# Kernel optimization log

Hardware: AMD Instinct MI355X
Metric: run time of the kernel (lower is better)

The kernel has to match this reference:

```python
import jax, jax.numpy as jnp
import numpy as np

BATCH, T, IN, HID = 64, 2048, 128, 256

def setup_inputs() -> dict:
    key = jax.random.key(0)
    ks = jax.random.split(key, 6)
    s = 0.05
    return {
        "x": jax.random.normal(ks[0], (BATCH, T, IN), dtype=jnp.float32),
        "w_ih0": jax.random.normal(ks[1], (IN, 4 * HID), dtype=jnp.float32) * s,
        "w_hh0": jax.random.normal(ks[2], (HID, 4 * HID), dtype=jnp.float32) * s,
        "b0": jnp.zeros((4 * HID,), dtype=jnp.float32),
        "w_ih1": jax.random.normal(ks[3], (HID, 4 * HID), dtype=jnp.float32) * s,
        "w_hh1": jax.random.normal(ks[4], (HID, 4 * HID), dtype=jnp.float32) * s,
        "b1": jnp.zeros((4 * HID,), dtype=jnp.float32),
    }

def _run_layer(xs, h0, c0, w_ih, w_hh, b):
    # xs: [T, B, D]. Original code iterates input_[T-1-t], i.e. reversed time.
    def step(carry, xt):
        h, c = carry
        gates = xt @ w_ih + h @ w_hh + b            # [B, 4H]
        f, i, o, g = jnp.split(gates, 4, axis=1)     # split order f,i,o,g as in source
        c1 = jax.nn.sigmoid(f) * c + jax.nn.sigmoid(i) * jnp.tanh(g)
        h1 = jax.nn.sigmoid(o) * jnp.tanh(c1)
        return (h1, c1), h1
    (hT, cT), ys = jax.lax.scan(step, (h0, c0), xs[::-1])
    return ys, hT, cT

def reference(x, w_ih0, w_hh0, b0, w_ih1, w_hh1, b1):
    xs = jnp.transpose(x, (1, 0, 2))                 # batch_first -> [T, B, IN]
    B = xs.shape[1]
    H = w_hh0.shape[0]
    h0 = jnp.zeros((B, H), dtype=xs.dtype)
    # Both layers start from the SAME zero hx (faithful to source).
    y0, hn0, cn0 = _run_layer(xs, h0, h0, w_ih0, w_hh0, b0)
    y1, hn1, cn1 = _run_layer(y0, h0, h0, w_ih1, w_hh1, b1)
    # Source never transposes output back: output is [T, B, H]
    return y1, (jnp.stack([hn0, hn1], 0), jnp.stack([cn0, cn1], 0))
```

## Files before the change

### kernel.cpp

```cpp
#include <hip/hip_runtime.h>
#include <cstdint>
#include <cstddef>

#define T_STEPS 2048
#define NBATCH  64
#define HID     256
#define NGATE   1024

#define KR   192
#define KRC  24
#define KLC  8
#define REC_LDS_BYTES (KLC*1024*16 + 1024)

typedef _Float16 f16x8 __attribute__((ext_vector_type(8)));
typedef _Float16 h2f   __attribute__((ext_vector_type(2)));
typedef float    f32x4 __attribute__((ext_vector_type(4)));

__device__ __forceinline__ unsigned short f2h_bits(float f) {
    _Float16 h = (_Float16)f;
    return __builtin_bit_cast(unsigned short, h);
}
__device__ __forceinline__ float h2f_scalar(unsigned short u) {
    return (float)__builtin_bit_cast(_Float16, u);
}

__device__ __forceinline__ float fdot2u(unsigned int hh, unsigned int ww, float acc) {
#if __has_builtin(__builtin_amdgcn_fdot2)
    return __builtin_amdgcn_fdot2(__builtin_bit_cast(h2f, hh),
                                  __builtin_bit_cast(h2f, ww), acc, false);
#else
    h2f a = __builtin_bit_cast(h2f, hh), b = __builtin_bit_cast(h2f, ww);
    return acc + (float)a.x * (float)b.x + (float)a.y * (float)b.y;
#endif
}

#define OFF_G    ((size_t)0)
#define OFF_Y0   ((size_t)268435456)
#define OFF_WT0  ((size_t)335544320)
#define OFF_WT1  ((size_t)336068608)
#define OFF_LW0  ((size_t)336592896)
#define OFF_LW1  ((size_t)336723968)
#define OFF_BS0  ((size_t)336855040)
#define OFF_BS1  ((size_t)337117184)
#define WS_NEED  ((size_t)337641472)

__global__ void convert_weights(const float* __restrict__ w_ih0, const float* __restrict__ w_hh0,
                                const float* __restrict__ w_ih1, const float* __restrict__ w_hh1,
                                unsigned short* __restrict__ WT0, unsigned short* __restrict__ WT1,
                                unsigned short* __restrict__ LW0, unsigned short* __restrict__ LW1,
                                unsigned short* __restrict__ BS0, unsigned short* __restrict__ BS1)
{
    int gid = blockIdx.x * blockDim.x + threadIdx.x;
    int gsz = gridDim.x * blockDim.x;
    for (int s = gid; s < 1024 * 256; s += gsz) {
        int j = s >> 8, k = s & 255;
        WT0[s] = f2h_bits(w_hh0[k * 1024 + j]);
        WT1[s] = f2h_bits(w_hh1[k * 1024 + j]);
    }
    for (int s = gid; s < KLC * 1024 * 8; s += gsz) {
        int i = s & 7, j = (s >> 3) & 1023, c = s >> 13;
        int k = KR + c * 8 + i;
        LW0[s] = f2h_bits(w_hh0[k * 1024 + j]);
        LW1[s] = f2h_bits(w_hh1[k * 1024 + j]);
    }
    for (int s = gid; s < 131072; s += gsz) {
        int i = s & 7, lane = (s >> 3) & 63, kb = (s >> 9) & 3, n16 = s >> 11;
        int k = kb * 32 + (lane >> 4) * 8 + i;
        int n = n16 * 16 + (lane & 15);
        BS0[s] = f2h_bits(w_ih0[k * 1024 + n]);
    }
    for (int s = gid; s < 262144; s += gsz) {
        int i = s & 7, lane = (s >> 3) & 63, kb = (s >> 9) & 7, n16 = s >> 12;
        int k = kb * 32 + (lane >> 4) * 8 + i;
        int n = n16 * 16 + (lane & 15);
        BS1[s] = f2h_bits(w_ih1[k * 1024 + n]);
    }
}

template <int KB, int LAYER>
__global__ __launch_bounds__(256) void gemm_in(const float* __restrict__ A32,
                                               const unsigned short* __restrict__ A16,
                                               const unsigned short* __restrict__ Bsw,
                                               const float* __restrict__ bias,
                                               unsigned short* __restrict__ Gout)
{
    const int lane = threadIdx.x & 63;
    const int wave = threadIdx.x >> 6;
    const int nblk = blockIdx.x & 15;
    const int rblk = blockIdx.x >> 4;
    const int r0 = rblk * 128 + wave * 32;
    const int quad = lane >> 4, ln = lane & 15;

    f32x4 acc[2][4];
#pragma unroll
    for (int q = 0; q < 4; q++) {
        float bv = bias[(nblk * 4 + q) * 16 + ln];
#pragma unroll
        for (int mt = 0; mt < 2; mt++) {
            acc[mt][q][0] = bv; acc[mt][q][1] = bv; acc[mt][q][2] = bv; acc[mt][q][3] = bv;
        }
    }
    const int ar0 = r0 + ln, ar1 = r0 + 16 + ln;
    size_t aoff0, aoff1;
    if (LAYER == 0) {
        aoff0 = ((size_t)(ar0 & 63) * 2048 + (size_t)(2047 - (ar0 >> 6))) * 128;
        aoff1 = ((size_t)(ar1 & 63) * 2048 + (size_t)(2047 - (ar1 >> 6))) * 128;
    } else {
        aoff0 = ((size_t)(2047 - (ar0 >> 6)) * 64 + (size_t)(ar0 & 63)) * 256;
        aoff1 = ((size_t)(2047 - (ar1 >> 6)) * 64 + (size_t)(ar1 & 63)) * 256;
    }
#pragma unroll
    for (int kb = 0; kb < KB; kb++) {
        const int k0 = kb * 32 + quad * 8;
        f16x8 a0, a1;
        if (LAYER == 0) {
            const float* p0 = A32 + aoff0 + k0;
            const float* p1 = A32 + aoff1 + k0;
            float4 fa = *(const float4*)(p0);
            float4 fb = *(const float4*)(p0 + 4);
            float4 fc = *(const float4*)(p1);
            float4 fd = *(const float4*)(p1 + 4);
            a0[0] = (_Float16)fa.x; a0[1] = (_Float16)fa.y; a0[2] = (_Float16)fa.z; a0[3] = (_Float16)fa.w;
            a0[4] = (_Float16)fb.x; a0[5] = (_Float16)fb.y; a0[6] = (_Float16)fb.z; a0[7] = (_Float16)fb.w;
            a1[0] = (_Float16)fc.x; a1[1] = (_Float16)fc.y; a1[2] = (_Float16)fc.z; a1[3] = (_Float16)fc.w;
            a1[4] = (_Float16)fd.x; a1[5] = (_Float16)fd.y; a1[6] = (_Float16)fd.z; a1[7] = (_Float16)fd.w;
        } else {
            a0 = *(const f16x8*)(A16 + aoff0 + k0);
            a1 = *(const f16x8*)(A16 + aoff1 + k0);
        }
#pragma unroll
        for (int q = 0; q < 4; q++) {
            f16x8 bq = *(const f16x8*)(Bsw + (((size_t)(nblk * 4 + q) * KB + kb) * 64 + lane) * 8);
            acc[0][q] = __builtin_amdgcn_mfma_f32_16x16x32_f16(a0, bq, acc[0][q], 0, 0, 0);
            acc[1][q] = __builtin_amdgcn_mfma_f32_16x16x32_f16(a1, bq, acc[1][q], 0, 0, 0);
        }
    }
#pragma unroll
    for (int mt = 0; mt < 2; mt++)
#pragma unroll
        for (int q = 0; q < 4; q++)
#pragma unroll
            for (int rg = 0; rg < 4; rg++) {
                int row = r0 + mt * 16 + quad * 4 + rg;
                int col = (nblk * 4 + q) * 16 + ln;
                int swz = ((col & 255) << 2) | (col >> 8);
                Gout[(size_t)row * 1024 + swz] = f2h_bits(acc[mt][q][rg]);
            }
}

template <int LAYER>
__global__ __launch_bounds__(512, 2) void lstm_rec(const unsigned short* __restrict__ G,
                                                   const unsigned short* __restrict__ WT,
                                                   const unsigned short* __restrict__ LW,
                                                   unsigned short* __restrict__ Y0,
                                                   float* __restrict__ Out)
{
    extern __shared__ char smem[];
    unsigned short* lds_w  = (unsigned short*)smem;
    unsigned short* lds_h0 = (unsigned short*)(smem + (size_t)KLC * 1024 * 16);
    unsigned short* lds_h1 = lds_h0 + 256;

    const int b = blockIdx.x;
    const int tid = threadIdx.x;
    const int wv = tid >> 6, l = tid & 63;
    const int upper = l >> 5;
    const int m = wv * 32 + (l & 31);
    const int j0 = m + upper * 512;
    const int j1 = j0 + 256;

    uint4 wr0[KRC], wr1[KRC];
    {
        const uint4* p0 = (const uint4*)(WT + (size_t)j0 * 256);
        const uint4* p1 = (const uint4*)(WT + (size_t)j1 * 256);
#pragma unroll
        for (int i = 0; i < KRC; i++) { wr0[i] = p0[i]; wr1[i] = p1[i]; }
    }
    {
        const uint4* src = (const uint4*)LW;
        uint4* dst = (uint4*)lds_w;
        for (int i = tid; i < KLC * 1024; i += 512) dst[i] = src[i];
    }
    if (tid < 256) lds_h0[tid] = 0;
    float c = 0.f, hprev = 0.f;
    __syncthreads();

    const unsigned int* Gb = (const unsigned int*)G + (size_t)b * 512;

    for (int t = 0; t < T_STEPS; ++t) {
        unsigned int gpack = Gb[(size_t)t * 32768 + m * 2 + upper];
        if (t && l < 32) {
            if (LAYER == 0) Y0[((size_t)(t - 1) * 64 + b) * 256 + m] = f2h_bits(hprev);
            else            Out[((size_t)(t - 1) * 64 + b) * 256 + m] = hprev;
        }
        const uint4* hv = (const uint4*)((t & 1) ? lds_h1 : lds_h0);
        float a00 = 0, a01 = 0, a02 = 0, a03 = 0;
        float a10 = 0, a11 = 0, a12 = 0, a13 = 0;
#pragma unroll
        for (int ci = 0; ci < KRC; ++ci) {
            uint4 h4 = hv[ci];
            uint4 w = wr0[ci];
            a00 = fdot2u(h4.x, w.x, a00); a01 = fdot2u(h4.y, w.y, a01);
            a02 = fdot2u(h4.z, w.z, a02); a03 = fdot2u(h4.w, w.w, a03);
            w = wr1[ci];
            a10 = fdot2u(h4.x, w.x, a10); a11 = fdot2u(h4.y, w.y, a11);
            a12 = fdot2u(h4.z, w.z, a12); a13 = fdot2u(h4.w, w.w, a13);
        }
        {
            const uint4* wl = (const uint4*)lds_w;
#pragma unroll
            for (int ci = 0; ci < KLC; ++ci) {
                uint4 h4 = hv[KRC + ci];
                uint4 w = wl[ci * 1024 + j0];
                a00 = fdot2u(h4.x, w.x, a00); a01 = fdot2u(h4.y, w.y, a01);
                a02 = fdot2u(h4.z, w.z, a02); a03 = fdot2u(h4.w, w.w, a03);
                w = wl[ci * 1024 + j1];
                a10 = fdot2u(h4.x, w.x, a10); a11 = fdot2u(h4.y, w.y, a11);
                a12 = fdot2u(h4.z, w.z, a12); a13 = fdot2u(h4.w, w.w, a13);
            }
        }
        float v0 = h2f_scalar((unsigned short)(gpack & 0xffff)) + ((a00 + a01) + (a02 + a03));
        float v1 = h2f_scalar((unsigned short)(gpack >> 16))    + ((a10 + a11) + (a12 + a13));
        float q0 = __shfl_xor(v0, 32, 64);
        float q1 = __shfl_xor(v1, 32, 64);
        float fg = upper ? q0 : v0;
        float ig = upper ? q1 : v1;
        float og = upper ? v0 : q0;
        float gg = upper ? v1 : q1;
        float sf = 1.f / (1.f + __expf(-fg));
        float si = 1.f / (1.f + __expf(-ig));
        float so = 1.f / (1.f + __expf(-og));
        float tg = 1.f - 2.f / (1.f + __expf(2.f * gg));
        c = sf * c + si * tg;
        float tc = 1.f - 2.f / (1.f + __expf(2.f * c));
        float h = so * tc;
        hprev = h;
        unsigned short* hn = (t & 1) ? lds_h0 : lds_h1;
        if (l < 32) hn[m] = f2h_bits(h);
        __syncthreads();
    }
    if (l < 32) {
        if (LAYER == 0) Y0[((size_t)(T_STEPS - 1) * 64 + b) * 256 + m] = f2h_bits(hprev);
        else            Out[((size_t)(T_STEPS - 1) * 64 + b) * 256 + m] = hprev;
        Out[(size_t)33554432 + (size_t)LAYER * 16384 + (size_t)b * 256 + m] = hprev;
        Out[(size_t)33554432 + 32768 + (size_t)LAYER * 16384 + (size_t)b * 256 + m] = c;
    }
}

extern "C" void kernel_launch(void* const* d_in, const int* in_sizes, int n_in,
                              void* d_out, int out_size, void* d_ws, size_t ws_size,
                              hipStream_t stream)
{
    const float* x     = (const float*)d_in[0];
    const float* w_ih0 = (const float*)d_in[1];
    const float* w_hh0 = (const float*)d_in[2];
    const float* b0    = (const float*)d_in[3];
    const float* w_ih1 = (const float*)d_in[4];
    const float* w_hh1 = (const float*)d_in[5];
    const float* b1    = (const float*)d_in[6];
    float* out = (float*)d_out;

    if (ws_size < WS_NEED) return;

    char* ws = (char*)d_ws;
    unsigned short* G   = (unsigned short*)(ws + OFF_G);
    unsigned short* Y0  = (unsigned short*)(ws + OFF_Y0);
    unsigned short* WT0 = (unsigned short*)(ws + OFF_WT0);
    unsigned short* WT1 = (unsigned short*)(ws + OFF_WT1);
    unsigned short* LW0 = (unsigned short*)(ws + OFF_LW0);
    unsigned short* LW1 = (unsigned short*)(ws + OFF_LW1);
    unsigned short* BS0 = (unsigned short*)(ws + OFF_BS0);
    unsigned short* BS1 = (unsigned short*)(ws + OFF_BS1);

    (void)hipFuncSetAttribute(reinterpret_cast<const void*>(&lstm_rec<0>),
                              hipFuncAttributeMaxDynamicSharedMemorySize, REC_LDS_BYTES);
    (void)hipFuncSetAttribute(reinterpret_cast<const void*>(&lstm_rec<1>),
                              hipFuncAttributeMaxDynamicSharedMemorySize, REC_LDS_BYTES);

    convert_weights<<<1024, 256, 0, stream>>>(w_ih0, w_hh0, w_ih1, w_hh1,
                                              WT0, WT1, LW0, LW1, BS0, BS1);
    gemm_in<4, 0><<<16384, 256, 0, stream>>>(x, nullptr, BS0, b0, G);
    lstm_rec<0><<<64, 512, REC_LDS_BYTES, stream>>>(G, WT0, LW0, Y0, out);
    gemm_in<8, 1><<<16384, 256, 0, stream>>>(nullptr, Y0, BS1, b1, G);
    lstm_rec<1><<<64, 512, REC_LDS_BYTES, stream>>>(G, WT1, LW1, Y0, out);
}
```

Baseline: 8.237 ms.

## Use MFMA for recurrent h·W_hh matvec instead of fdot2 loops

Replaces the per-thread fdot2 dot products in the recurrent step with 16x16x32 f16 MFMA instructions. The h vector is broadcast as the A operand, so only row 0 of each tile is useful. Weights are re-laid out into MFMA B-fragment order, with 6 of 8 K-tiles held in registers and 2 in LDS. It also prefetches the next step's gate preactivations one step ahead. The aim is to shorten the serial per-step latency, at the cost of wasted MFMA rows and more register pressure.

```diff
diff --git a/kernel.cpp b/kernel.cpp
--- a/kernel.cpp
+++ b/kernel.cpp
@@ -7,14 +7,11 @@
 #define HID     256
 #define NGATE   1024
 
-#define KR   192
-#define KRC  24
-#define KLC  8
-#define REC_LDS_BYTES (KLC*1024*16 + 1024)
+#define REC_LDS_BYTES (128*1024 + 1024)
 
 typedef _Float16 f16x8 __attribute__((ext_vector_type(8)));
-typedef _Float16 h2f   __attribute__((ext_vector_type(2)));
 typedef float    f32x4 __attribute__((ext_vector_type(4)));
+typedef unsigned short u16x4 __attribute__((ext_vector_type(4)));
 
 __device__ __forceinline__ unsigned short f2h_bits(float f) {
     _Float16 h = (_Float16)f;
@@ -24,44 +21,44 @@
     return (float)__builtin_bit_cast(_Float16, u);
 }
 
-__device__ __forceinline__ float fdot2u(unsigned int hh, unsigned int ww, float acc) {
-#if __has_builtin(__builtin_amdgcn_fdot2)
-    return __builtin_amdgcn_fdot2(__builtin_bit_cast(h2f, hh),
-                                  __builtin_bit_cast(h2f, ww), acc, false);
-#else
-    h2f a = __builtin_bit_cast(h2f, hh), b = __builtin_bit_cast(h2f, ww);
-    return acc + (float)a.x * (float)b.x + (float)a.y * (float)b.y;
-#endif
-}
-
 #define OFF_G    ((size_t)0)
 #define OFF_Y0   ((size_t)268435456)
-#define OFF_WT0  ((size_t)335544320)
-#define OFF_WT1  ((size_t)336068608)
-#define OFF_LW0  ((size_t)336592896)
-#define OFF_LW1  ((size_t)336723968)
-#define OFF_BS0  ((size_t)336855040)
-#define OFF_BS1  ((size_t)337117184)
-#define WS_NEED  ((size_t)337641472)
+#define OFF_RW0  ((size_t)335544320)
+#define OFF_RW1  ((size_t)335937536)
+#define OFF_LF0  ((size_t)336330752)
+#define OFF_LF1  ((size_t)336461824)
+#define OFF_BS0  ((size_t)336592896)
+#define OFF_BS1  ((size_t)336855040)
+#define WS_NEED  ((size_t)337379328)
 
 __global__ void convert_weights(const float* __restrict__ w_ih0, const float* __restrict__ w_hh0,
                                 const float* __restrict__ w_ih1, const float* __restrict__ w_hh1,
-                                unsigned short* __restrict__ WT0, unsigned short* __restrict__ WT1,
-                                unsigned short* __restrict__ LW0, unsigned short* __restrict__ LW1,
+                                unsigned short* __restrict__ RW0, unsigned short* __restrict__ RW1,
+                                unsigned short* __restrict__ LF0, unsigned short* __restrict__ LF1,
                                 unsigned short* __restrict__ BS0, unsigned short* __restrict__ BS1)
 {
     int gid = blockIdx.x * blockDim.x + threadIdx.x;
     int gsz = gridDim.x * blockDim.x;
-    for (int s = gid; s < 1024 * 256; s += gsz) {
-        int j = s >> 8, k = s & 255;
-        WT0[s] = f2h_bits(w_hh0[k * 1024 + j]);
-        WT1[s] = f2h_bits(w_hh1[k * 1024 + j]);
-    }
-    for (int s = gid; s < KLC * 1024 * 8; s += gsz) {
-        int i = s & 7, j = (s >> 3) & 1023, c = s >> 13;
-        int k = KR + c * 8 + i;
-        LW0[s] = f2h_bits(w_hh0[k * 1024 + j]);
-        LW1[s] = f2h_bits(w_hh1[k * 1024 + j]);
+    for (int s = gid; s < 196608; s += gsz) {
+        int i = s & 7, l = (s >> 3) & 63;
+        int rest = s >> 9;
+        int kt = rest % 6, m2 = rest / 6;
+        int t8 = m2 & 7, wv = m2 >> 3;
+        int col0 = (t8 >> 1) * 256 + wv * 32 + (t8 & 1) * 16;
+        int k = kt * 32 + (l >> 4) * 8 + i;
+        int col = col0 + (l & 15);
+        RW0[s] = f2h_bits(w_hh0[k * 1024 + col]);
+        RW1[s] = f2h_bits(w_hh1[k * 1024 + col]);
+    }
+    for (int s = gid; s < 65536; s += gsz) {
+        int i = s & 7, l = (s >> 3) & 63;
+        int rest = s >> 9;
+        int kc = rest & 1, t8 = (rest >> 1) & 7, wv = rest >> 4;
+        int col0 = (t8 >> 1) * 256 + wv * 32 + (t8 & 1) * 16;
+        int k = (6 + kc) * 32 + (l >> 4) * 8 + i;
+        int col = col0 + (l & 15);
+        LF0[s] = f2h_bits(w_hh0[k * 1024 + col]);
+        LF1[s] = f2h_bits(w_hh1[k * 1024 + col]);
     }
     for (int s = gid; s < 131072; s += gsz) {
         int i = s & 7, lane = (s >> 3) & 63, kb = (s >> 9) & 3, n16 = s >> 11;
@@ -150,99 +147,132 @@
 
 template <int LAYER>
 __global__ __launch_bounds__(512, 2) void lstm_rec(const unsigned short* __restrict__ G,
-                                                   const unsigned short* __restrict__ WT,
-                                                   const unsigned short* __restrict__ LW,
+                                                   const unsigned short* __restrict__ RW,
+                                                   const unsigned short* __restrict__ LF,
                                                    unsigned short* __restrict__ Y0,
                                                    float* __restrict__ Out)
 {
     extern __shared__ char smem[];
     unsigned short* lds_w  = (unsigned short*)smem;
-    unsigned short* lds_h0 = (unsigned short*)(smem + (size_t)KLC * 1024 * 16);
+    unsigned short* lds_h0 = (unsigned short*)(smem + 128 * 1024);
     unsigned short* lds_h1 = lds_h0 + 256;
 
     const int b = blockIdx.x;
     const int tid = threadIdx.x;
     const int wv = tid >> 6, l = tid & 63;
-    const int upper = l >> 5;
-    const int m = wv * 32 + (l & 31);
-    const int j0 = m + upper * 512;
-    const int j1 = j0 + 256;
-
-    uint4 wr0[KRC], wr1[KRC];
+    const int q = l >> 4, ln = l & 15;
+    const int u_low = wv * 32 + ln;
+    const int u_high = u_low + 16;
+
+    f16x8 rw[8][6];
+#pragma unroll
+    for (int t8 = 0; t8 < 8; ++t8)
+#pragma unroll
+        for (int kt = 0; kt < 6; ++kt)
+            rw[t8][kt] = *(const f16x8*)(RW + (((size_t)(wv * 8 + t8) * 6 + kt) * 64 + l) * 8);
+
     {
-        const uint4* p0 = (const uint4*)(WT + (size_t)j0 * 256);
-        const uint4* p1 = (const uint4*)(WT + (size_t)j1 * 256);
-#pragma unroll
-        for (int i = 0; i < KRC; i++) { wr0[i] = p0[i]; wr1[i] = p1[i]; }
-    }
-    {
-        const uint4* src = (const uint4*)LW;
+        const uint4* src = (const uint4*)LF;
         uint4* dst = (uint4*)lds_w;
-        for (int i = tid; i < KLC * 1024; i += 512) dst[i] = src[i];
+        for (int i = tid; i < 8192; i += 512) dst[i] = src[i];
     }
     if (tid < 256) lds_h0[tid] = 0;
-    float c = 0.f, hprev = 0.f;
+    float c_l = 0.f, c_h = 0.f, hp_l = 0.f, hp_h = 0.f;
     __syncthreads();
 
-    const unsigned int* Gb = (const unsigned int*)G + (size_t)b * 512;
+    const u16x4* Gp = (const u16x4*)G;
+    const size_t gbl = (size_t)b * 256 + u_low;
+    const size_t gbh = gbl + 16;
+    u16x4 gl = Gp[gbl];
+    u16x4 gh = Gp[gbh];
 
     for (int t = 0; t < T_STEPS; ++t) {
-        unsigned int gpack = Gb[(size_t)t * 32768 + m * 2 + upper];
-        if (t && l < 32) {
-            if (LAYER == 0) Y0[((size_t)(t - 1) * 64 + b) * 256 + m] = f2h_bits(hprev);
-            else            Out[((size_t)(t - 1) * 64 + b) * 256 + m] = hprev;
-        }
-        const uint4* hv = (const uint4*)((t & 1) ? lds_h1 : lds_h0);
-        float a00 = 0, a01 = 0, a02 = 0, a03 = 0;
-        float a10 = 0, a11 = 0, a12 = 0, a13 = 0;
-#pragma unroll
-        for (int ci = 0; ci < KRC; ++ci) {
-            uint4 h4 = hv[ci];
-            uint4 w = wr0[ci];
-            a00 = fdot2u(h4.x, w.x, a00); a01 = fdot2u(h4.y, w.y, a01);
-            a02 = fdot2u(h4.z, w.z, a02); a03 = fdot2u(h4.w, w.w, a03);
-            w = wr1[ci];
-            a10 = fdot2u(h4.x, w.x, a10); a11 = fdot2u(h4.y, w.y, a11);
-            a12 = fdot2u(h4.z, w.z, a12); a13 = fdot2u(h4.w, w.w, a13);
+        const int tn = (t + 1 < T_STEPS) ? t + 1 : t;
+        u16x4 gln = Gp[(size_t)tn * 16384 + gbl];
+        u16x4 ghn = Gp[(size_t)tn * 16384 + gbh];
+        if (t && q == 0) {
+            if (LAYER == 0) {
+                Y0[((size_t)(t - 1) * 64 + b) * 256 + u_low]  = f2h_bits(hp_l);
+                Y0[((size_t)(t - 1) * 64 + b) * 256 + u_high] = f2h_bits(hp_h);
+            } else {
+                Out[((size_t)(t - 1) * 64 + b) * 256 + u_low]  = hp_l;
+                Out[((size_t)(t - 1) * 64 + b) * 256 + u_high] = hp_h;
+            }
+        }
+        const unsigned short* hbuf = (t & 1) ? lds_h1 : lds_h0;
+
+        float svf_l, svf_h, svi_l, svi_h;
+        float so_l, so_h, sg_l, sg_h;
+#pragma unroll
+        for (int p = 0; p < 2; ++p) {
+            f32x4 acc[4];
+#pragma unroll
+            for (int j = 0; j < 4; ++j) {
+                unsigned short gv = (j & 1) ? gh[p * 2 + (j >> 1)] : gl[p * 2 + (j >> 1)];
+                acc[j][0] = h2f_scalar(gv);
+                acc[j][1] = 0.f; acc[j][2] = 0.f; acc[j][3] = 0.f;
+            }
+#pragma unroll
+            for (int kt = 0; kt < 8; ++kt) {
+                f16x8 av = *(const f16x8*)(hbuf + kt * 32 + q * 8);
+#pragma unroll
+                for (int j = 0; j < 4; ++j) {
+                    const int t8 = p * 4 + j;
+                    f16x8 bv;
+                    if (kt < 6) {
+                        bv = rw[t8][kt];
+                    } else {
+                        bv = *(const f16x8*)(lds_w + (((size_t)(wv * 8 + t8) * 2 + (kt - 6)) * 64 + l) * 8);
+                    }
+                    acc[j] = __builtin_amdgcn_mfma_f32_16x16x32_f16(av, bv, acc[j], 0, 0, 0);
+                }
+            }
+            if (p == 0) {
+                svf_l = acc[0][0]; svf_h = acc[1][0];
+                svi_l = acc[2][0]; svi_h = acc[3][0];
+            } else {
+                so_l = acc[0][0]; so_h = acc[1][0];
+                sg_l = acc[2][0]; sg_h = acc[3][0];
+            }
         }
         {
-            const uint4* wl = (const uint4*)lds_w;
-#pragma unroll
-            for (int ci = 0; ci < KLC; ++ci) {
-                uint4 h4 = hv[KRC + ci];
-                uint4 w = wl[ci * 1024 + j0];
-                a00 = fdot2u(h4.x, w.x, a00); a01 = fdot2u(h4.y, w.y, a01);
-                a02 = fdot2u(h4.z, w.z, a02); a03 = fdot2u(h4.w, w.w, a03);
-                w = wl[ci * 1024 + j1];
-                a10 = fdot2u(h4.x, w.x, a10); a11 = fdot2u(h4.y, w.y, a11);
-                a12 = fdot2u(h4.z, w.z, a12); a13 = fdot2u(h4.w, w.w, a13);
-            }
-        }
-        float v0 = h2f_scalar((unsigned short)(gpack & 0xffff)) + ((a00 + a01) + (a02 + a03));
-        float v1 = h2f_scalar((unsigned short)(gpack >> 16))    + ((a10 + a11) + (a12 + a13));
-        float q0 = __shfl_xor(v0, 32, 64);
-        float q1 = __shfl_xor(v1, 32, 64);
-        float fg = upper ? q0 : v0;
-        float ig = upper ? q1 : v1;
-        float og = upper ? v0 : q0;
-        float gg = upper ? v1 : q1;
-        float sf = 1.f / (1.f + __expf(-fg));
-        float si = 1.f / (1.f + __expf(-ig));
-        float so = 1.f / (1.f + __expf(-og));
-        float tg = 1.f - 2.f / (1.f + __expf(2.f * gg));
-        c = sf * c + si * tg;
-        float tc = 1.f - 2.f / (1.f + __expf(2.f * c));
-        float h = so * tc;
-        hprev = h;
+            float sf = 1.f / (1.f + __expf(-svf_l));
+            float si = 1.f / (1.f + __expf(-svi_l));
+            float so = 1.f / (1.f + __expf(-so_l));
+            float tg = 1.f - 2.f / (1.f + __expf(2.f * sg_l));
+            c_l = sf * c_l + si * tg;
+            float tc = 1.f - 2.f / (1.f + __expf(2.f * c_l));
+            hp_l = so * tc;
+        }
+        {
+            float sf = 1.f / (1.f + __expf(-svf_h));
+            float si = 1.f / (1.f + __expf(-svi_h));
+            float so = 1.f / (1.f + __expf(-so_h));
+            float tg = 1.f - 2.f / (1.f + __expf(2.f * sg_h));
+            c_h = sf * c_h + si * tg;
+            float tc = 1.f - 2.f / (1.f + __expf(2.f * c_h));
+            hp_h = so * tc;
+        }
         unsigned short* hn = (t & 1) ? lds_h0 : lds_h1;
-        if (l < 32) hn[m] = f2h_bits(h);
+        if (q == 0) {
+            hn[u_low]  = f2h_bits(hp_l);
+            hn[u_high] = f2h_bits(hp_h);
+        }
+        gl = gln; gh = ghn;
         __syncthreads();
     }
-    if (l < 32) {
-        if (LAYER == 0) Y0[((size_t)(T_STEPS - 1) * 64 + b) * 256 + m] = f2h_bits(hprev);
-        else            Out[((size_t)(T_STEPS - 1) * 64 + b) * 256 + m] = hprev;
-        Out[(size_t)33554432 + (size_t)LAYER * 16384 + (size_t)b * 256 + m] = hprev;
-        Out[(size_t)33554432 + 32768 + (size_t)LAYER * 16384 + (size_t)b * 256 + m] = c;
+    if (q == 0) {
+        if (LAYER == 0) {
+            Y0[((size_t)(T_STEPS - 1) * 64 + b) * 256 + u_low]  = f2h_bits(hp_l);
+            Y0[((size_t)(T_STEPS - 1) * 64 + b) * 256 + u_high] = f2h_bits(hp_h);
+        } else {
+            Out[((size_t)(T_STEPS - 1) * 64 + b) * 256 + u_low]  = hp_l;
+            Out[((size_t)(T_STEPS - 1) * 64 + b) * 256 + u_high] = hp_h;
+        }
+        Out[(size_t)33554432 + (size_t)LAYER * 16384 + (size_t)b * 256 + u_low]  = hp_l;
+        Out[(size_t)33554432 + (size_t)LAYER * 16384 + (size_t)b * 256 + u_high] = hp_h;
+        Out[(size_t)33554432 + 32768 + (size_t)LAYER * 16384 + (size_t)b * 256 + u_low]  = c_l;
+        Out[(size_t)33554432 + 32768 + (size_t)LAYER * 16384 + (size_t)b * 256 + u_high] = c_h;
     }
 }
 
@@ -264,10 +294,10 @@
     char* ws = (char*)d_ws;
     unsigned short* G   = (unsigned short*)(ws + OFF_G);
     unsigned short* Y0  = (unsigned short*)(ws + OFF_Y0);
-    unsigned short* WT0 = (unsigned short*)(ws + OFF_WT0);
-    unsigned short* WT1 = (unsigned short*)(ws + OFF_WT1);
-    unsigned short* LW0 = (unsigned short*)(ws + OFF_LW0);
-    unsigned short* LW1 = (unsigned short*)(ws + OFF_LW1);
+    unsigned short* RW0 = (unsigned short*)(ws + OFF_RW0);
+    unsigned short* RW1 = (unsigned short*)(ws + OFF_RW1);
+    unsigned short* LF0 = (unsigned short*)(ws + OFF_LF0);
+    unsigned short* LF1 = (unsigned short*)(ws + OFF_LF1);
     unsigned short* BS0 = (unsigned short*)(ws + OFF_BS0);
     unsigned short* BS1 = (unsigned short*)(ws + OFF_BS1);
 
@@ -277,9 +307,9 @@
                               hipFuncAttributeMaxDynamicSharedMemorySize, REC_LDS_BYTES);
 
     convert_weights<<<1024, 256, 0, stream>>>(w_ih0, w_hh0, w_ih1, w_hh1,
-                                              WT0, WT1, LW0, LW1, BS0, BS1);
+                                              RW0, RW1, LF0, LF1, BS0, BS1);
     gemm_in<4, 0><<<16384, 256, 0, stream>>>(x, nullptr, BS0, b0, G);
-    lstm_rec<0><<<64, 512, REC_LDS_BYTES, stream>>>(G, WT0, LW0, Y0, out);
+    lstm_rec<0><<<64, 512, REC_LDS_BYTES, stream>>>(G, RW0, LF0, Y0, out);
     gemm_in<8, 1><<<16384, 256, 0, stream>>>(nullptr, Y0, BS1, b1, G);
-    lstm_rec<1><<<64, 512, REC_LDS_BYTES, stream>>>(G, WT1, LW1, Y0, out);
-}
+    lstm_rec<1><<<64, 512, REC_LDS_BYTES, stream>>>(G, RW1, LF1, Y0, out);
+}
```

Measured after the change: 12.18 ms. 1.48x slower.

## Split recurrent K across wave pairs with readlane broadcast and LDS partial-sum exchange

Applied to the files above, without the earlier changes.

Reorganises the recurrent matvec so each thread owns one hidden unit's four gates over half of K, with two waves per unit group splitting K and exchanging partial sums through LDS. The h vector is broadcast to SGPRs with readlane instead of being reread from LDS per chunk, and the weight layout is repacked to match. The next step's gate preactivations are prefetched one step ahead. This removes per-step LDS reads of h and the cross-lane shuffle, at the cost of an extra barrier per step, 64 readlanes per step and a larger LDS footprint.

```diff
diff --git a/kernel.cpp b/kernel.cpp
--- a/kernel.cpp
+++ b/kernel.cpp
@@ -7,14 +7,12 @@
 #define HID     256
 #define NGATE   1024
 
-#define KR   192
-#define KRC  24
-#define KLC  8
-#define REC_LDS_BYTES (KLC*1024*16 + 1024)
+#define REC_LDS_BYTES (128*1024 + 8192 + 1024)
 
 typedef _Float16 f16x8 __attribute__((ext_vector_type(8)));
 typedef _Float16 h2f   __attribute__((ext_vector_type(2)));
 typedef float    f32x4 __attribute__((ext_vector_type(4)));
+typedef unsigned short u16x4 __attribute__((ext_vector_type(4)));
 
 __device__ __forceinline__ unsigned short f2h_bits(float f) {
     _Float16 h = (_Float16)f;
@@ -36,32 +34,49 @@
 
 #define OFF_G    ((size_t)0)
 #define OFF_Y0   ((size_t)268435456)
-#define OFF_WT0  ((size_t)335544320)
-#define OFF_WT1  ((size_t)336068608)
-#define OFF_LW0  ((size_t)336592896)
-#define OFF_LW1  ((size_t)336723968)
-#define OFF_BS0  ((size_t)336855040)
-#define OFF_BS1  ((size_t)337117184)
-#define WS_NEED  ((size_t)337641472)
+#define OFF_RW0  ((size_t)335544320)
+#define OFF_RW1  ((size_t)335937536)
+#define OFF_LF0  ((size_t)336330752)
+#define OFF_LF1  ((size_t)336461824)
+#define OFF_BS0  ((size_t)336592896)
+#define OFF_BS1  ((size_t)336855040)
+#define WS_NEED  ((size_t)337379328)
 
 __global__ void convert_weights(const float* __restrict__ w_ih0, const float* __restrict__ w_hh0,
                                 const float* __restrict__ w_ih1, const float* __restrict__ w_hh1,
-                                unsigned short* __restrict__ WT0, unsigned short* __restrict__ WT1,
-                                unsigned short* __restrict__ LW0, unsigned short* __restrict__ LW1,
+                                unsigned short* __restrict__ RW0, unsigned short* __restrict__ RW1,
+                                unsigned short* __restrict__ LF0, unsigned short* __restrict__ LF1,
                                 unsigned short* __restrict__ BS0, unsigned short* __restrict__ BS1)
 {
     int gid = blockIdx.x * blockDim.x + threadIdx.x;
     int gsz = gridDim.x * blockDim.x;
-    for (int s = gid; s < 1024 * 256; s += gsz) {
-        int j = s >> 8, k = s & 255;
-        WT0[s] = f2h_bits(w_hh0[k * 1024 + j]);
-        WT1[s] = f2h_bits(w_hh1[k * 1024 + j]);
-    }
-    for (int s = gid; s < KLC * 1024 * 8; s += gsz) {
-        int i = s & 7, j = (s >> 3) & 1023, c = s >> 13;
-        int k = KR + c * 8 + i;
-        LW0[s] = f2h_bits(w_hh0[k * 1024 + j]);
-        LW1[s] = f2h_bits(w_hh1[k * 1024 + j]);
+    for (int s = gid; s < 196608; s += gsz) {
+        int i = s & 7;
+        int t = s >> 3;
+        int slot = t & 511;
+        int q = t >> 9;
+        int g = q / 12, c = q % 12;
+        int l = slot & 63, wv = slot >> 6;
+        int kh = wv & 1, ug = wv >> 1;
+        int jp = c * 4 + (i >> 1);
+        int k = kh * 128 + jp * 2 + (i & 1);
+        int col = g * 256 + ug * 64 + l;
+        RW0[s] = f2h_bits(w_hh0[k * 1024 + col]);
+        RW1[s] = f2h_bits(w_hh1[k * 1024 + col]);
+    }
+    for (int s = gid; s < 65536; s += gsz) {
+        int i = s & 7;
+        int t = s >> 3;
+        int slot = t & 511;
+        int r = t >> 9;
+        int g = r >> 2, cc = r & 3;
+        int l = slot & 63, wv = slot >> 6;
+        int kh = wv & 1, ug = wv >> 1;
+        int jp = 48 + cc * 4 + (i >> 1);
+        int k = kh * 128 + jp * 2 + (i & 1);
+        int col = g * 256 + ug * 64 + l;
+        LF0[s] = f2h_bits(w_hh0[k * 1024 + col]);
+        LF1[s] = f2h_bits(w_hh1[k * 1024 + col]);
     }
     for (int s = gid; s < 131072; s += gsz) {
         int i = s & 7, lane = (s >> 3) & 63, kb = (s >> 9) & 3, n16 = s >> 11;
@@ -150,99 +165,118 @@
 
 template <int LAYER>
 __global__ __launch_bounds__(512, 2) void lstm_rec(const unsigned short* __restrict__ G,
-                                                   const unsigned short* __restrict__ WT,
-                                                   const unsigned short* __restrict__ LW,
+                                                   const unsigned short* __restrict__ RW,
+                                                   const unsigned short* __restrict__ LF,
                                                    unsigned short* __restrict__ Y0,
                                                    float* __restrict__ Out)
 {
     extern __shared__ char smem[];
-    unsigned short* lds_w  = (unsigned short*)smem;
-    unsigned short* lds_h0 = (unsigned short*)(smem + (size_t)KLC * 1024 * 16);
+    uint4*  lds_w  = (uint4*)smem;
+    float4* pb     = (float4*)(smem + 131072);
+    unsigned short* lds_h0 = (unsigned short*)(smem + 131072 + 8192);
     unsigned short* lds_h1 = lds_h0 + 256;
 
     const int b = blockIdx.x;
     const int tid = threadIdx.x;
     const int wv = tid >> 6, l = tid & 63;
-    const int upper = l >> 5;
-    const int m = wv * 32 + (l & 31);
-    const int j0 = m + upper * 512;
-    const int j1 = j0 + 256;
-
-    uint4 wr0[KRC], wr1[KRC];
+    const int kh = wv & 1;
+    const int ug = wv >> 1;
+    const int m = ug * 64 + l;
+
+    uint4 rw[4][12];
+#pragma unroll
+    for (int g = 0; g < 4; ++g)
+#pragma unroll
+        for (int c = 0; c < 12; ++c)
+            rw[g][c] = *(const uint4*)(RW + ((size_t)((g * 12 + c) * 512) + tid) * 8);
+
     {
-        const uint4* p0 = (const uint4*)(WT + (size_t)j0 * 256);
-        const uint4* p1 = (const uint4*)(WT + (size_t)j1 * 256);
-#pragma unroll
-        for (int i = 0; i < KRC; i++) { wr0[i] = p0[i]; wr1[i] = p1[i]; }
-    }
-    {
-        const uint4* src = (const uint4*)LW;
-        uint4* dst = (uint4*)lds_w;
-        for (int i = tid; i < KLC * 1024; i += 512) dst[i] = src[i];
+        const uint4* src = (const uint4*)LF;
+        for (int i = tid; i < 8192; i += 512) lds_w[i] = src[i];
     }
     if (tid < 256) lds_h0[tid] = 0;
-    float c = 0.f, hprev = 0.f;
+    float c_state = 0.f, hprev = 0.f;
     __syncthreads();
 
-    const unsigned int* Gb = (const unsigned int*)G + (size_t)b * 512;
+    const u16x4* Gp = (const u16x4*)G;
+    const size_t gbase = (size_t)b * 256 + m;
+    u16x4 gp = Gp[gbase];
 
     for (int t = 0; t < T_STEPS; ++t) {
-        unsigned int gpack = Gb[(size_t)t * 32768 + m * 2 + upper];
-        if (t && l < 32) {
+        const uint4* hv4 = (const uint4*)((t & 1) ? lds_h1 : lds_h0);
+        uint4 hq = hv4[kh * 16 + (l & 15)];
+
+        const int tn = (t + 1 < T_STEPS) ? t + 1 : t;
+        u16x4 gpn = Gp[(size_t)tn * 16384 + gbase];
+
+        if (t && kh == 0) {
             if (LAYER == 0) Y0[((size_t)(t - 1) * 64 + b) * 256 + m] = f2h_bits(hprev);
             else            Out[((size_t)(t - 1) * 64 + b) * 256 + m] = hprev;
         }
-        const uint4* hv = (const uint4*)((t & 1) ? lds_h1 : lds_h0);
-        float a00 = 0, a01 = 0, a02 = 0, a03 = 0;
-        float a10 = 0, a11 = 0, a12 = 0, a13 = 0;
-#pragma unroll
-        for (int ci = 0; ci < KRC; ++ci) {
-            uint4 h4 = hv[ci];
-            uint4 w = wr0[ci];
-            a00 = fdot2u(h4.x, w.x, a00); a01 = fdot2u(h4.y, w.y, a01);
-            a02 = fdot2u(h4.z, w.z, a02); a03 = fdot2u(h4.w, w.w, a03);
-            w = wr1[ci];
-            a10 = fdot2u(h4.x, w.x, a10); a11 = fdot2u(h4.y, w.y, a11);
-            a12 = fdot2u(h4.z, w.z, a12); a13 = fdot2u(h4.w, w.w, a13);
-        }
-        {
-            const uint4* wl = (const uint4*)lds_w;
-#pragma unroll
-            for (int ci = 0; ci < KLC; ++ci) {
-                uint4 h4 = hv[KRC + ci];
-                uint4 w = wl[ci * 1024 + j0];
-                a00 = fdot2u(h4.x, w.x, a00); a01 = fdot2u(h4.y, w.y, a01);
-                a02 = fdot2u(h4.z, w.z, a02); a03 = fdot2u(h4.w, w.w, a03);
-                w = wl[ci * 1024 + j1];
-                a10 = fdot2u(h4.x, w.x, a10); a11 = fdot2u(h4.y, w.y, a11);
-                a12 = fdot2u(h4.z, w.z, a12); a13 = fdot2u(h4.w, w.w, a13);
+
+        unsigned hx = hq.x, hy = hq.y, hz = hq.z, hw = hq.w;
+        unsigned sh[64];
+#pragma unroll
+        for (int q = 0; q < 16; ++q) {
+            sh[q * 4 + 0] = __builtin_amdgcn_readlane(hx, q);
+            sh[q * 4 + 1] = __builtin_amdgcn_readlane(hy, q);
+            sh[q * 4 + 2] = __builtin_amdgcn_readlane(hz, q);
+            sh[q * 4 + 3] = __builtin_amdgcn_readlane(hw, q);
+        }
+
+        float acc[4] = {0.f, 0.f, 0.f, 0.f};
+#pragma unroll
+        for (int c = 0; c < 12; ++c) {
+#pragma unroll
+            for (int g = 0; g < 4; ++g) {
+                uint4 w = rw[g][c];
+                acc[g] = fdot2u(sh[c * 4 + 0], w.x, acc[g]);
+                acc[g] = fdot2u(sh[c * 4 + 1], w.y, acc[g]);
+                acc[g] = fdot2u(sh[c * 4 + 2], w.z, acc[g]);
+                acc[g] = fdot2u(sh[c * 4 + 3], w.w, acc[g]);
             }
         }
-        float v0 = h2f_scalar((unsigned short)(gpack & 0xffff)) + ((a00 + a01) + (a02 + a03));
-        float v1 = h2f_scalar((unsigned short)(gpack >> 16))    + ((a10 + a11) + (a12 + a13));
-        float q0 = __shfl_xor(v0, 32, 64);
-        float q1 = __shfl_xor(v1, 32, 64);
-        float fg = upper ? q0 : v0;
-        float ig = upper ? q1 : v1;
-        float og = upper ? v0 : q0;
-        float gg = upper ? v1 : q1;
+#pragma unroll
+        for (int cc = 0; cc < 4; ++cc) {
+#pragma unroll
+            for (int g = 0; g < 4; ++g) {
+                uint4 w = lds_w[(g * 4 + cc) * 512 + tid];
+                acc[g] = fdot2u(sh[48 + cc * 4 + 0], w.x, acc[g]);
+                acc[g] = fdot2u(sh[48 + cc * 4 + 1], w.y, acc[g]);
+                acc[g] = fdot2u(sh[48 + cc * 4 + 2], w.z, acc[g]);
+                acc[g] = fdot2u(sh[48 + cc * 4 + 3], w.w, acc[g]);
+            }
+        }
+
+        float4 pv; pv.x = acc[0]; pv.y = acc[1]; pv.z = acc[2]; pv.w = acc[3];
+        pb[tid] = pv;
+        __syncthreads();
+        float4 pp = pb[tid ^ 64];
+
+        float fg = h2f_scalar(gp[0]) + (acc[0] + pp.x);
+        float ig = h2f_scalar(gp[1]) + (acc[1] + pp.y);
+        float og = h2f_scalar(gp[2]) + (acc[2] + pp.z);
+        float gg = h2f_scalar(gp[3]) + (acc[3] + pp.w);
+
         float sf = 1.f / (1.f + __expf(-fg));
         float si = 1.f / (1.f + __expf(-ig));
         float so = 1.f / (1.f + __expf(-og));
         float tg = 1.f - 2.f / (1.f + __expf(2.f * gg));
-        c = sf * c + si * tg;
-        float tc = 1.f - 2.f / (1.f + __expf(2.f * c));
+        c_state = sf * c_state + si * tg;
+        float tc = 1.f - 2.f / (1.f + __expf(2.f * c_state));
         float h = so * tc;
         hprev = h;
+
         unsigned short* hn = (t & 1) ? lds_h0 : lds_h1;
-        if (l < 32) hn[m] = f2h_bits(h);
+        if (kh == 0) hn[m] = f2h_bits(h);
+        gp = gpn;
         __syncthreads();
     }
-    if (l < 32) {
+    if (kh == 0) {
         if (LAYER == 0) Y0[((size_t)(T_STEPS - 1) * 64 + b) * 256 + m] = f2h_bits(hprev);
         else            Out[((size_t)(T_STEPS - 1) * 64 + b) * 256 + m] = hprev;
         Out[(size_t)33554432 + (size_t)LAYER * 16384 + (size_t)b * 256 + m] = hprev;
-        Out[(size_t)33554432 + 32768 + (size_t)LAYER * 16384 + (size_t)b * 256 + m] = c;
+        Out[(size_t)33554432 + 32768 + (size_t)LAYER * 16384 + (size_t)b * 256 + m] = c_state;
     }
 }
 
@@ -264,10 +298,10 @@
     char* ws = (char*)d_ws;
     unsigned short* G   = (unsigned short*)(ws + OFF_G);
     unsigned short* Y0  = (unsigned short*)(ws + OFF_Y0);
-    unsigned short* WT0 = (unsigned short*)(ws + OFF_WT0);
-    unsigned short* WT1 = (unsigned short*)(ws + OFF_WT1);
-    unsigned short* LW0 = (unsigned short*)(ws + OFF_LW0);
-    unsigned short* LW1 = (unsigned short*)(ws + OFF_LW1);
+    unsigned short* RW0 = (unsigned short*)(ws + OFF_RW0);
+    unsigned short* RW1 = (unsigned short*)(ws + OFF_RW1);
+    unsigned short* LF0 = (unsigned short*)(ws + OFF_LF0);
+    unsigned short* LF1 = (unsigned short*)(ws + OFF_LF1);
     unsigned short* BS0 = (unsigned short*)(ws + OFF_BS0);
     unsigned short* BS1 = (unsigned short*)(ws + OFF_BS1);
 
@@ -277,9 +311,9 @@
                               hipFuncAttributeMaxDynamicSharedMemorySize, REC_LDS_BYTES);
 
     convert_weights<<<1024, 256, 0, stream>>>(w_ih0, w_hh0, w_ih1, w_hh1,
-                                              WT0, WT1, LW0, LW1, BS0, BS1);
+                                              RW0, RW1, LF0, LF1, BS0, BS1);
     gemm_in<4, 0><<<16384, 256, 0, stream>>>(x, nullptr, BS0, b0, G);
-    lstm_rec<0><<<64, 512, REC_LDS_BYTES, stream>>>(G, WT0, LW0, Y0, out);
+    lstm_rec<0><<<64, 512, REC_LDS_BYTES, stream>>>(G, RW0, LF0, Y0, out);
     gemm_in<8, 1><<<16384, 256, 0, stream>>>(nullptr, Y0, BS1, b1, G);
-    lstm_rec<1><<<64, 512, REC_LDS_BYTES, stream>>>(G, WT1, LW1, Y0, out);
-}
+    lstm_rec<1><<<64, 512, REC_LDS_BYTES, stream>>>(G, RW1, LF1, Y0, out);
+}
```

Measured after the change: 7.957 ms. -3.4%, faster.
